# Kernel tuning notes

Measured on AMD Instinct MI355X. Metric: run time of the kernel, lower is better.

The kernel has to match this reference:

```python
import jax, jax.numpy as jnp
import numpy as np

N = 50000      # num nodes
E = 20000      # num hyperedges
NNZ = 800000   # incidence entries
F_IN = 256
HID = [256, 256]
EPS = 1e-5     # BatchNorm eps


def setup_inputs() -> dict:
    key = jax.random.key(0)
    ks = jax.random.split(key, 12)
    x = jax.random.normal(ks[0], (N, F_IN), jnp.float32)
    node_idx = jax.random.randint(ks[1], (NNZ,), 0, N, dtype=jnp.int32)
    edge_idx = jax.random.randint(ks[2], (NNZ,), 0, E, dtype=jnp.int32)
    hyperedge_index = jnp.stack([node_idx, edge_idx])  # [2, NNZ]
    hyperedge_weight = jax.random.uniform(ks[3], (E,), jnp.float32, 0.1, 1.0)
    # layer params: Linear(in, out, bias) + BatchNorm(gamma, beta)
    W1 = jax.random.normal(ks[4], (F_IN, HID[0]), jnp.float32) * (1.0 / np.sqrt(F_IN))
    b1 = jax.random.normal(ks[5], (HID[0],), jnp.float32) * 0.02
    g1 = jnp.ones((HID[0],), jnp.float32)
    be1 = jnp.zeros((HID[0],), jnp.float32)
    W2 = jax.random.normal(ks[6], (HID[0], HID[1]), jnp.float32) * (1.0 / np.sqrt(HID[0]))
    b2 = jax.random.normal(ks[7], (HID[1],), jnp.float32) * 0.02
    g2 = jnp.ones((HID[1],), jnp.float32)
    be2 = jnp.zeros((HID[1],), jnp.float32)
    return dict(x=x, hyperedge_index=hyperedge_index, hyperedge_weight=hyperedge_weight,
                W1=W1, b1=b1, g1=g1, be1=be1, W2=W2, b2=b2, g2=g2, be2=be2)


def _hypergraph_layer(x, node_idx, edge_idx, w_e, W, b, g, be):
    """One HypergraphLayer: HypergraphConv (no attention, heads=1) + BN(train) + ReLU.

    PyG HypergraphConv math: out = D^{-1} H B^{-1} H^T (X Theta) + bias,
    where D_i = sum of incident hyperedge weights, B_e = hyperedge cardinality.
    """
    x = x @ W                                   # [N, F_out] node transform
    # node degree weighted by hyperedge weight
    D = jax.ops.segment_sum(w_e[edge_idx], node_idx, num_segments=N)
    Dinv = jnp.where(D != 0, 1.0 / D, 0.0)
    # hyperedge cardinality
    B = jax.ops.segment_sum(jnp.ones((NNZ,), x.dtype), edge_idx, num_segments=E)
    Binv = jnp.where(B != 0, 1.0 / B, 0.0)
    # node -> edge aggregation: e = B^{-1} H^T x
    e = Binv[:, None] * jax.ops.segment_sum(x[node_idx], edge_idx, num_segments=E)
    # edge -> node aggregation: out = D^{-1} H e
    out = Dinv[:, None] * jax.ops.segment_sum(e[edge_idx], node_idx, num_segments=N)
    out = out + b
    # BatchNorm1d (training mode: biased batch stats over the node dim)
    mu = out.mean(axis=0)
    var = out.var(axis=0)
    out = (out - mu) * jax.lax.rsqrt(var + EPS) * g + be
    return jax.nn.relu(out)                     # dropout p=0.0 -> identity


def reference(x, hyperedge_index, hyperedge_weight, W1, b1, g1, be1, W2, b2, g2, be2):
    node_idx = hyperedge_index[0]
    edge_idx = hyperedge_index[1]
    h = _hypergraph_layer(x, node_idx, edge_idx, hyperedge_weight, W1, b1, g1, be1)
    h = _hypergraph_layer(h, node_idx, edge_idx, hyperedge_weight, W2, b2, g2, be2)
    return h
```

## Files before the change

kernel.cpp:

```cpp
#include <hip/hip_runtime.h>

#define NN     50000
#define NE     20000
#define NNZV   800000
#define FD     256
#define EPSV   1e-5f
#define MPAD   20032
#define NCOPY  32
#define BE     ((NE + 255) / 256)
#define BN     ((NN + 255) / 256)

typedef __attribute__((ext_vector_type(8))) __bf16 bf16x8;
typedef __attribute__((ext_vector_type(4))) __bf16 bf16x4;
typedef __attribute__((ext_vector_type(4))) float f32x4;

__device__ __forceinline__ float b2f(unsigned short u) {
  union { unsigned int i; float f; } z; z.i = ((unsigned)u) << 16; return z.f;
}


__global__ void hg_hist(const int* __restrict__ nidx, const int* __restrict__ eidx,
                        const float* __restrict__ wedge,
                        int* __restrict__ cntc_e, int* __restrict__ cntc_n,
                        float* __restrict__ Daccc,
                        int* __restrict__ rank_e, int* __restrict__ rank_n) {
  int i = blockIdx.x * 256 + threadIdx.x;
  if (i >= NNZV) return;
  int copy = blockIdx.x & (NCOPY - 1);
  int e = eidx[i];
  int n = nidx[i];
  rank_e[i] = atomicAdd(&cntc_e[copy * NE + e], 1);
  rank_n[i] = atomicAdd(&cntc_n[copy * NN + n], 1);
  atomicAdd(&Daccc[copy * NN + n], wedge[e]);
}

__global__ void hg_colreduce_e(int* __restrict__ cntc_e, int* __restrict__ total_e,
                               float* __restrict__ Binv) {
  int e = blockIdx.x * 256 + threadIdx.x;
  if (e >= NE) return;
  int run = 0;
#pragma unroll
  for (int c = 0; c < NCOPY; ++c) {
    int v = cntc_e[c * NE + e];
    cntc_e[c * NE + e] = run;
    run += v;
  }
  total_e[e] = run;
  Binv[e] = run ? 1.0f / (float)run : 0.0f;
}

__global__ void hg_colreduce_n(int* __restrict__ cntc_n, const float* __restrict__ Daccc,
                               int* __restrict__ total_n, float* __restrict__ Dinv) {
  int n = blockIdx.x * 256 + threadIdx.x;
  if (n >= NN) return;
  int run = 0;
  float d = 0.f;
#pragma unroll
  for (int c = 0; c < NCOPY; ++c) {
    int v = cntc_n[c * NN + n];
    cntc_n[c * NN + n] = run;
    run += v;
    d += Daccc[c * NN + n];
  }
  total_n[n] = run;
  Dinv[n] = (d != 0.f) ? 1.0f / d : 0.0f;
}


__global__ void hg_scan1(const int* __restrict__ total_e, const int* __restrict__ total_n,
                         int* __restrict__ part) {
  __shared__ int lds[256];
  int b = blockIdx.x;
  const int* src;
  int n, idx0;
  if (b < BE) { src = total_e; n = NE; idx0 = b * 256; }
  else        { src = total_n; n = NN; idx0 = (b - BE) * 256; }
  int t = threadIdx.x;
  int idx = idx0 + t;
  lds[t] = (idx < n) ? src[idx] : 0;
  for (int d = 128; d > 0; d >>= 1) {
    __syncthreads();
    if (t < d) lds[t] += lds[t + d];
  }
  if (t == 0) part[b] = lds[0];
}

__global__ void hg_scan2(int* __restrict__ part, int* __restrict__ off_e,
                         int* __restrict__ off_n) {
  __shared__ int lds[256];
  int t = threadIdx.x;
  int v = (t < BE) ? part[t] : 0;
  lds[t] = v;
  for (int d = 1; d < 256; d <<= 1) {
    __syncthreads();
    int u = (t >= d) ? lds[t - d] : 0;
    int w = lds[t];
    __syncthreads();
    lds[t] = u + w;
  }
  __syncthreads();
  if (t < BE) part[t] = lds[t] - v;
  if (t == 255) off_e[NE] = lds[255];
  __syncthreads();
  v = (t < BN) ? part[BE + t] : 0;
  lds[t] = v;
  for (int d = 1; d < 256; d <<= 1) {
    __syncthreads();
    int u = (t >= d) ? lds[t - d] : 0;
    int w = lds[t];
    __syncthreads();
    lds[t] = u + w;
  }
  __syncthreads();
  if (t < BN) part[BE + t] = lds[t] - v;
  if (t == 255) off_n[NN] = lds[255];
}

__global__ void hg_scan3(const int* __restrict__ total_e, const int* __restrict__ total_n,
                         const int* __restrict__ part,
                         int* __restrict__ off_e, int* __restrict__ off_n) {
  __shared__ int lds[256];
  int b = blockIdx.x;
  const int* src;
  int* dst;
  int n, idx0;
  if (b < BE) { src = total_e; dst = off_e; n = NE; idx0 = b * 256; }
  else        { src = total_n; dst = off_n; n = NN; idx0 = (b - BE) * 256; }
  int base = part[b];
  int t = threadIdx.x;
  int idx = idx0 + t;
  int v = (idx < n) ? src[idx] : 0;
  lds[t] = v;
  for (int d = 1; d < 256; d <<= 1) {
    __syncthreads();
    int u = (t >= d) ? lds[t - d] : 0;
    int w = lds[t];
    __syncthreads();
    lds[t] = u + w;
  }
  __syncthreads();
  if (idx < n) dst[idx] = base + lds[t] - v;
}

__global__ void hg_addoff(int* __restrict__ cntc_e, int* __restrict__ cntc_n,
                          const int* __restrict__ off_e, const int* __restrict__ off_n) {
  int id = blockIdx.x * 256 + threadIdx.x;
  if (id < NCOPY * NE) {
    cntc_e[id] += off_e[id % NE];
  } else {
    id -= NCOPY * NE;
    if (id < NCOPY * NN) cntc_n[id] += off_n[id % NN];
  }
}

__global__ void hg_scatter(const int* __restrict__ nidx, const int* __restrict__ eidx,
                           const int* __restrict__ cntc_e, const int* __restrict__ cntc_n,
                           const int* __restrict__ rank_e, const int* __restrict__ rank_n,
                           int* __restrict__ mem_e, int* __restrict__ mem_n) {
  int i = blockIdx.x * 256 + threadIdx.x;
  if (i >= NNZV) return;
  int copy = blockIdx.x & (NCOPY - 1);
  int e = eidx[i];
  int n = nidx[i];
  mem_e[cntc_e[copy * NE + e] + rank_e[i]] = n;
  mem_n[cntc_n[copy * NN + n] + rank_n[i]] = e;
}


__global__ void hg_wconv(const float* __restrict__ W1, const float* __restrict__ W2,
                         __bf16* __restrict__ Wt1, __bf16* __restrict__ Wt2) {
  int id = blockIdx.x * 256 + threadIdx.x;
  int n = id >> 8;
  int k = id & 255;
  Wt1[n * FD + k] = (__bf16)W1[k * FD + n];
  Wt2[n * FD + k] = (__bf16)W2[k * FD + n];
}


__global__ void hg_x2bf(const float* __restrict__ X, __bf16* __restrict__ Xbf) {
  int idx = blockIdx.x * 256 + threadIdx.x;
  if (idx >= NN * FD / 4) return;
  float4 v = ((const float4*)X)[idx];
  bf16x4 o = {(__bf16)v.x, (__bf16)v.y, (__bf16)v.z, (__bf16)v.w};
  ((bf16x4*)Xbf)[idx] = o;
}


template<int APPLY>
__global__ __launch_bounds__(256) void
hg_agg_n2e_bf(const __bf16* __restrict__ Xbf, const int* __restrict__ off_e,
              const int* __restrict__ mem_e, const float* __restrict__ Binv,
              const float* __restrict__ scale, const float* __restrict__ shift,
              __bf16* __restrict__ Ebf) {
  int wid = blockIdx.x * 4 + (threadIdx.x >> 6);
  if (wid >= NE) return;
  int lane = threadIdx.x & 63;
  int c = lane * 4;
  float4 sc = {0.f, 0.f, 0.f, 0.f}, sh = {0.f, 0.f, 0.f, 0.f};
  if (APPLY) {
    sc = *(const float4*)(scale + c);
    sh = *(const float4*)(shift + c);
  }
  const unsigned short* Xu = (const unsigned short*)Xbf;
  int lo = off_e[wid], hi = off_e[wid + 1];
  float a0 = 0.f, a1 = 0.f, a2 = 0.f, a3 = 0.f;

#define ACC4(v) do { \
    float f0 = b2f((v).x), f1 = b2f((v).y), f2 = b2f((v).z), f3 = b2f((v).w); \
    if (APPLY) { \
      f0 = fmaxf(fmaf(f0, sc.x, sh.x), 0.f); \
      f1 = fmaxf(fmaf(f1, sc.y, sh.y), 0.f); \
      f2 = fmaxf(fmaf(f2, sc.z, sh.z), 0.f); \
      f3 = fmaxf(fmaf(f3, sc.w, sh.w), 0.f); \
    } \
    a0 += f0; a1 += f1; a2 += f2; a3 += f3; } while (0)

  int m = lo;
  for (; m + 4 <= hi; m += 4) {
    int i0 = mem_e[m], i1 = mem_e[m + 1], i2 = mem_e[m + 2], i3 = mem_e[m + 3];
    ushort4 v0 = *(const ushort4*)(Xu + (size_t)i0 * FD + c);
    ushort4 v1 = *(const ushort4*)(Xu + (size_t)i1 * FD + c);
    ushort4 v2 = *(const ushort4*)(Xu + (size_t)i2 * FD + c);
    ushort4 v3 = *(const ushort4*)(Xu + (size_t)i3 * FD + c);
    ACC4(v0); ACC4(v1); ACC4(v2); ACC4(v3);
  }
  for (; m < hi; ++m) {
    int i0 = mem_e[m];
    ushort4 v0 = *(const ushort4*)(Xu + (size_t)i0 * FD + c);
    ACC4(v0);
  }
  float bi = Binv[wid];
  bf16x4 o = {(__bf16)(a0 * bi), (__bf16)(a1 * bi), (__bf16)(a2 * bi), (__bf16)(a3 * bi)};
  *(bf16x4*)(Ebf + (size_t)wid * FD + c) = o;
}


__global__ void hg_gemm(const __bf16* __restrict__ A, const __bf16* __restrict__ Bt,
                        __bf16* __restrict__ C, int Mrows) {
  int tid = threadIdx.x;
  int w = tid >> 6;
  int l = tid & 63;
  int m0 = blockIdx.x * 64 + w * 16;
  int n0 = blockIdx.y * 16;
  int kbase = (l >> 4) * 8;
  const bf16x8* Ap = (const bf16x8*)(A + (size_t)(m0 + (l & 15)) * FD + kbase);
  const bf16x8* Bp = (const bf16x8*)(Bt + (size_t)(n0 + (l & 15)) * FD + kbase);
  f32x4 acc = {0.f, 0.f, 0.f, 0.f};
#pragma unroll
  for (int ks = 0; ks < 8; ++ks) {
    bf16x8 a = Ap[ks * 4];
    bf16x8 b = Bp[ks * 4];
    acc = __builtin_amdgcn_mfma_f32_16x16x32_bf16(a, b, acc, 0, 0, 0);
  }
  int crow = m0 + (l >> 4) * 4;
  int ccol = n0 + (l & 15);
#pragma unroll
  for (int r = 0; r < 4; ++r) {
    int rr = crow + r;
    if (rr < Mrows) C[(size_t)rr * FD + ccol] = (__bf16)acc[r];
  }
}


__global__ __launch_bounds__(256) void
hg_agg_e2n_bf(const __bf16* __restrict__ eWbf, const int* __restrict__ off_n,
              const int* __restrict__ mem_n, const float* __restrict__ Dinv,
              const float* __restrict__ bias, __bf16* __restrict__ Outbf) {
  int node = blockIdx.x * 4 + (threadIdx.x >> 6);
  if (node >= NN) return;
  int lane = threadIdx.x & 63;
  int c = lane * 4;
  const unsigned short* eWu = (const unsigned short*)eWbf;
  int lo = off_n[node], hi = off_n[node + 1];
  float a0 = 0.f, a1 = 0.f, a2 = 0.f, a3 = 0.f;
  int m = lo;
  for (; m + 4 <= hi; m += 4) {
    int i0 = mem_n[m], i1 = mem_n[m + 1], i2 = mem_n[m + 2], i3 = mem_n[m + 3];
    ushort4 v0 = *(const ushort4*)(eWu + (size_t)i0 * FD + c);
    ushort4 v1 = *(const ushort4*)(eWu + (size_t)i1 * FD + c);
    ushort4 v2 = *(const ushort4*)(eWu + (size_t)i2 * FD + c);
    ushort4 v3 = *(const ushort4*)(eWu + (size_t)i3 * FD + c);
    a0 += b2f(v0.x); a1 += b2f(v0.y); a2 += b2f(v0.z); a3 += b2f(v0.w);
    a0 += b2f(v1.x); a1 += b2f(v1.y); a2 += b2f(v1.z); a3 += b2f(v1.w);
    a0 += b2f(v2.x); a1 += b2f(v2.y); a2 += b2f(v2.z); a3 += b2f(v2.w);
    a0 += b2f(v3.x); a1 += b2f(v3.y); a2 += b2f(v3.z); a3 += b2f(v3.w);
  }
  for (; m < hi; ++m) {
    int i0 = mem_n[m];
    ushort4 v0 = *(const ushort4*)(eWu + (size_t)i0 * FD + c);
    a0 += b2f(v0.x); a1 += b2f(v0.y); a2 += b2f(v0.z); a3 += b2f(v0.w);
  }
  float di = Dinv[node];
  float4 b4 = *(const float4*)(bias + c);
  bf16x4 o = {(__bf16)fmaf(a0, di, b4.x), (__bf16)fmaf(a1, di, b4.y),
              (__bf16)fmaf(a2, di, b4.z), (__bf16)fmaf(a3, di, b4.w)};
  *(bf16x4*)(Outbf + (size_t)node * FD + c) = o;
}


__global__ __launch_bounds__(256) void
hg_stats(const __bf16* __restrict__ Outbf, float* __restrict__ stats) {
  int c = threadIdx.x;
  int rpb = (NN + gridDim.x - 1) / gridDim.x;
  int r0 = blockIdx.x * rpb;
  int r1 = r0 + rpb;
  if (r1 > NN) r1 = NN;
  const unsigned short* Ou = (const unsigned short*)Outbf;
  float s = 0.f, q = 0.f;
  for (int r = r0; r < r1; ++r) {
    float v = b2f(Ou[(size_t)r * FD + c]);
    s += v;
    q = fmaf(v, v, q);
  }
  atomicAdd(&stats[c], s);
  atomicAdd(&stats[FD + c], q);
}


__global__ void hg_bn_finalize(const float* __restrict__ stats, const float* __restrict__ g,
                               const float* __restrict__ be,
                               float* __restrict__ scale, float* __restrict__ shift) {
  int c = threadIdx.x;
  float mu = stats[c] * (1.0f / NN);
  float var = stats[FD + c] * (1.0f / NN) - mu * mu;
  float sc = g[c] * rsqrtf(var + EPSV);
  scale[c] = sc;
  shift[c] = fmaf(-mu, sc, be[c]);
}

__global__ void hg_apply_bf(const __bf16* __restrict__ Outbf, const float* __restrict__ scale,
                            const float* __restrict__ shift, float* __restrict__ H) {
  int idx = blockIdx.x * 256 + threadIdx.x;
  if (idx >= NN * FD / 8) return;
  ushort4 v0 = ((const ushort4*)Outbf)[idx * 2 + 0];
  ushort4 v1 = ((const ushort4*)Outbf)[idx * 2 + 1];
  int c = (idx & (FD / 8 - 1)) * 8;
  float4 sa = *(const float4*)(scale + c);
  float4 sb = *(const float4*)(scale + c + 4);
  float4 ha = *(const float4*)(shift + c);
  float4 hb = *(const float4*)(shift + c + 4);
  float4 o0, o1;
  o0.x = fmaxf(fmaf(b2f(v0.x), sa.x, ha.x), 0.f);
  o0.y = fmaxf(fmaf(b2f(v0.y), sa.y, ha.y), 0.f);
  o0.z = fmaxf(fmaf(b2f(v0.z), sa.z, ha.z), 0.f);
  o0.w = fmaxf(fmaf(b2f(v0.w), sa.w, ha.w), 0.f);
  o1.x = fmaxf(fmaf(b2f(v1.x), sb.x, hb.x), 0.f);
  o1.y = fmaxf(fmaf(b2f(v1.y), sb.y, hb.y), 0.f);
  o1.z = fmaxf(fmaf(b2f(v1.z), sb.z, hb.z), 0.f);
  o1.w = fmaxf(fmaf(b2f(v1.w), sb.w, hb.w), 0.f);
  ((float4*)H)[idx * 2 + 0] = o0;
  ((float4*)H)[idx * 2 + 1] = o1;
}


extern "C" void kernel_launch(void* const* d_in, const int* in_sizes, int n_in,
                              void* d_out, int out_size, void* d_ws, size_t ws_size,
                              hipStream_t stream) {
  const float* x    = (const float*)d_in[0];
  const int*   hei  = (const int*)d_in[1];
  const int*   nidx = hei;
  const int*   eidx = hei + NNZV;
  const float* wedge = (const float*)d_in[2];
  const float* W1  = (const float*)d_in[3];
  const float* b1  = (const float*)d_in[4];
  const float* g1  = (const float*)d_in[5];
  const float* be1 = (const float*)d_in[6];
  const float* W2  = (const float*)d_in[7];
  const float* b2  = (const float*)d_in[8];
  const float* g2  = (const float*)d_in[9];
  const float* be2 = (const float*)d_in[10];
  float* out = (float*)d_out;

  char* base = (char*)d_ws;
  size_t cur = 0;
  auto alloc = [&](size_t bytes) -> void* {
    void* p = base + cur;
    cur += (bytes + 255) & ~(size_t)255;
    return p;
  };
  int*   cntc_e = (int*)alloc((size_t)NCOPY * NE * 4);
  int*   cntc_n = (int*)alloc((size_t)NCOPY * NN * 4);
  float* Daccc  = (float*)alloc((size_t)NCOPY * NN * 4);
  size_t zero_span = cur;
  int*   rank_e = (int*)alloc((size_t)NNZV * 4);
  int*   rank_n = (int*)alloc((size_t)NNZV * 4);
  int*   total_e = (int*)alloc(NE * 4);
  int*   total_n = (int*)alloc(NN * 4);
  int*   part   = (int*)alloc((BE + BN) * 4);
  int*   off_e = (int*)alloc((NE + 1) * 4);
  int*   off_n = (int*)alloc((NN + 1) * 4);
  int*   mem_e = (int*)alloc((size_t)NNZV * 4);
  int*   mem_n = (int*)alloc((size_t)NNZV * 4);
  float* Dinv  = (float*)alloc(NN * 4);
  float* Binv  = (float*)alloc(NE * 4);
  __bf16* Wt1  = (__bf16*)alloc(FD * FD * 2);
  __bf16* Wt2  = (__bf16*)alloc(FD * FD * 2);
  __bf16* Xbf  = (__bf16*)alloc((size_t)NN * FD * 2);
  __bf16* Ebf  = (__bf16*)alloc((size_t)MPAD * FD * 2);
  __bf16* eWbf = (__bf16*)alloc((size_t)MPAD * FD * 2);
  __bf16* Outbf = (__bf16*)alloc((size_t)NN * FD * 2);
  float* stats = (float*)alloc(2 * FD * 4);
  float* scale1 = (float*)alloc(FD * 4);
  float* shift1 = (float*)alloc(FD * 4);
  float* scale2 = (float*)alloc(FD * 4);
  float* shift2 = (float*)alloc(FD * 4);
  if (cur > ws_size) return;

  hipMemsetAsync(base, 0, zero_span, stream);

  hg_hist<<<(NNZV + 255) / 256, 256, 0, stream>>>(nidx, eidx, wedge, cntc_e, cntc_n,
                                                  Daccc, rank_e, rank_n);
  hg_colreduce_e<<<(NE + 255) / 256, 256, 0, stream>>>(cntc_e, total_e, Binv);
  hg_colreduce_n<<<(NN + 255) / 256, 256, 0, stream>>>(cntc_n, Daccc, total_n, Dinv);
  hg_scan1<<<BE + BN, 256, 0, stream>>>(total_e, total_n, part);
  hg_scan2<<<1, 256, 0, stream>>>(part, off_e, off_n);
  hg_scan3<<<BE + BN, 256, 0, stream>>>(total_e, total_n, part, off_e, off_n);
  hg_addoff<<<(NCOPY * (NE + NN) + 255) / 256, 256, 0, stream>>>(cntc_e, cntc_n, off_e, off_n);
  hg_scatter<<<(NNZV + 255) / 256, 256, 0, stream>>>(nidx, eidx, cntc_e, cntc_n,
                                                     rank_e, rank_n, mem_e, mem_n);
  hg_wconv<<<FD, 256, 0, stream>>>(W1, W2, Wt1, Wt2);
  hg_x2bf<<<(NN * FD / 4 + 255) / 256, 256, 0, stream>>>(x, Xbf);

  const int N2E_BLOCKS = (NE + 3) / 4;
  const int E2N_BLOCKS = (NN + 3) / 4;

  hg_agg_n2e_bf<0><<<N2E_BLOCKS, 256, 0, stream>>>(Xbf, off_e, mem_e, Binv,
                                                   nullptr, nullptr, Ebf);
  hg_gemm<<<dim3(MPAD / 64, FD / 16), 256, 0, stream>>>(Ebf, Wt1, eWbf, NE);
  hg_agg_e2n_bf<<<E2N_BLOCKS, 256, 0, stream>>>(eWbf, off_n, mem_n, Dinv, b1, Outbf);
  hipMemsetAsync(stats, 0, 2 * FD * 4, stream);
  hg_stats<<<256, 256, 0, stream>>>(Outbf, stats);
  hg_bn_finalize<<<1, FD, 0, stream>>>(stats, g1, be1, scale1, shift1);

  hg_agg_n2e_bf<1><<<N2E_BLOCKS, 256, 0, stream>>>(Outbf, off_e, mem_e, Binv,
                                                   scale1, shift1, Ebf);
  hg_gemm<<<dim3(MPAD / 64, FD / 16), 256, 0, stream>>>(Ebf, Wt2, eWbf, NE);
  hg_agg_e2n_bf<<<E2N_BLOCKS, 256, 0, stream>>>(eWbf, off_n, mem_n, Dinv, b2, Outbf);
  hipMemsetAsync(stats, 0, 2 * FD * 4, stream);
  hg_stats<<<256, 256, 0, stream>>>(Outbf, stats);
  hg_bn_finalize<<<1, FD, 0, stream>>>(stats, g2, be2, scale2, shift2);
  hg_apply_bf<<<(NN * FD / 8 + 255) / 256, 256, 0, stream>>>(Outbf, scale2, shift2, out);
}
```

Baseline: 688.6 us.

## Build CSR with LDS-packed 16-bit histograms and compute degrees on the fly

Replaces the global-atomic multi-copy histogram with a per-block LDS histogram that packs two 16-bit counters per word, over 128 contiguous chunks. Ranks are stored as 16-bit values, and the per-copy offset is added inside scatter, which removes the memset and addoff kernels. Binv and Dinv are no longer precomputed: they come from the CSR segment length and a running sum of hyperedge weights inside the aggregation kernels. The aggregation loops are also unrolled to 8 gathers. The trade-off is a few extra wedge gathers in the e2n kernel, and 16-bit counters that overflow if any chunk sees 65536 or more repeats of one id.

```diff
diff --git a/kernel.cpp b/kernel.cpp
--- a/kernel.cpp
+++ b/kernel.cpp
@@ -6,7 +6,11 @@
 #define FD     256
 #define EPSV   1e-5f
 #define MPAD   20032
-#define NCOPY  32
+#define NCPY   128
+#define EPB    (NNZV / NCPY)
+#define HEC    (NE / 2)
+#define HNC    (NN / 2)
+#define HTC    (HEC + HNC)
 #define BE     ((NE + 255) / 256)
 #define BN     ((NN + 255) / 256)
 
@@ -19,51 +23,49 @@
 }
 
 
-__global__ void hg_hist(const int* __restrict__ nidx, const int* __restrict__ eidx,
-                        const float* __restrict__ wedge,
-                        int* __restrict__ cntc_e, int* __restrict__ cntc_n,
-                        float* __restrict__ Daccc,
-                        int* __restrict__ rank_e, int* __restrict__ rank_n) {
-  int i = blockIdx.x * 256 + threadIdx.x;
-  if (i >= NNZV) return;
-  int copy = blockIdx.x & (NCOPY - 1);
-  int e = eidx[i];
-  int n = nidx[i];
-  rank_e[i] = atomicAdd(&cntc_e[copy * NE + e], 1);
-  rank_n[i] = atomicAdd(&cntc_n[copy * NN + n], 1);
-  atomicAdd(&Daccc[copy * NN + n], wedge[e]);
-}
-
-__global__ void hg_colreduce_e(int* __restrict__ cntc_e, int* __restrict__ total_e,
-                               float* __restrict__ Binv) {
-  int e = blockIdx.x * 256 + threadIdx.x;
-  if (e >= NE) return;
-  int run = 0;
-#pragma unroll
-  for (int c = 0; c < NCOPY; ++c) {
-    int v = cntc_e[c * NE + e];
-    cntc_e[c * NE + e] = run;
+__global__ __launch_bounds__(256) void
+hg_histlds(const int* __restrict__ nidx, const int* __restrict__ eidx,
+           unsigned* __restrict__ cntc,
+           unsigned short* __restrict__ rank_e16, unsigned short* __restrict__ rank_n16) {
+  __shared__ unsigned hist[HTC];
+  int b = blockIdx.x, t = threadIdx.x;
+  for (int j = t; j < HTC; j += 256) hist[j] = 0;
+  __syncthreads();
+  int i0 = b * EPB;
+  for (int i = i0 + t; i < i0 + EPB; i += 256) {
+    int e = eidx[i];
+    int n = nidx[i];
+    unsigned se = (e & 1) * 16;
+    unsigned sn = (n & 1) * 16;
+    unsigned oe = atomicAdd(&hist[e >> 1], 1u << se);
+    unsigned on = atomicAdd(&hist[HEC + (n >> 1)], 1u << sn);
+    rank_e16[i] = (unsigned short)((oe >> se) & 0xffffu);
+    rank_n16[i] = (unsigned short)((on >> sn) & 0xffffu);
+  }
+  __syncthreads();
+  unsigned* dst = cntc + (size_t)b * HTC;
+  for (int j = t; j < HTC; j += 256) dst[j] = hist[j];
+}
+
+__global__ void hg_colreduce(unsigned* __restrict__ cntc,
+                             int* __restrict__ total_e, int* __restrict__ total_n) {
+  int j = blockIdx.x * 256 + threadIdx.x;
+  if (j >= HTC) return;
+  unsigned run = 0;
+#pragma unroll 4
+  for (int c = 0; c < NCPY; ++c) {
+    unsigned v = cntc[(size_t)c * HTC + j];
+    cntc[(size_t)c * HTC + j] = run;
     run += v;
   }
-  total_e[e] = run;
-  Binv[e] = run ? 1.0f / (float)run : 0.0f;
-}
-
-__global__ void hg_colreduce_n(int* __restrict__ cntc_n, const float* __restrict__ Daccc,
-                               int* __restrict__ total_n, float* __restrict__ Dinv) {
-  int n = blockIdx.x * 256 + threadIdx.x;
-  if (n >= NN) return;
-  int run = 0;
-  float d = 0.f;
-#pragma unroll
-  for (int c = 0; c < NCOPY; ++c) {
-    int v = cntc_n[c * NN + n];
-    cntc_n[c * NN + n] = run;
-    run += v;
-    d += Daccc[c * NN + n];
-  }
-  total_n[n] = run;
-  Dinv[n] = (d != 0.f) ? 1.0f / d : 0.0f;
+  if (j < HEC) {
+    total_e[2 * j]     = run & 0xffffu;
+    total_e[2 * j + 1] = run >> 16;
+  } else {
+    int k = j - HEC;
+    total_n[2 * k]     = run & 0xffffu;
+    total_n[2 * k + 1] = run >> 16;
+  }
 }
 
 
@@ -142,28 +144,24 @@
   if (idx < n) dst[idx] = base + lds[t] - v;
 }
 
-__global__ void hg_addoff(int* __restrict__ cntc_e, int* __restrict__ cntc_n,
-                          const int* __restrict__ off_e, const int* __restrict__ off_n) {
-  int id = blockIdx.x * 256 + threadIdx.x;
-  if (id < NCOPY * NE) {
-    cntc_e[id] += off_e[id % NE];
-  } else {
-    id -= NCOPY * NE;
-    if (id < NCOPY * NN) cntc_n[id] += off_n[id % NN];
-  }
-}
 
 __global__ void hg_scatter(const int* __restrict__ nidx, const int* __restrict__ eidx,
-                           const int* __restrict__ cntc_e, const int* __restrict__ cntc_n,
-                           const int* __restrict__ rank_e, const int* __restrict__ rank_n,
+                           const unsigned* __restrict__ cntc,
+                           const unsigned short* __restrict__ rank_e16,
+                           const unsigned short* __restrict__ rank_n16,
+                           const int* __restrict__ off_e, const int* __restrict__ off_n,
                            int* __restrict__ mem_e, int* __restrict__ mem_n) {
   int i = blockIdx.x * 256 + threadIdx.x;
   if (i >= NNZV) return;
-  int copy = blockIdx.x & (NCOPY - 1);
+  unsigned copy = (unsigned)i / EPB;
   int e = eidx[i];
   int n = nidx[i];
-  mem_e[cntc_e[copy * NE + e] + rank_e[i]] = n;
-  mem_n[cntc_n[copy * NN + n] + rank_n[i]] = e;
+  unsigned be = cntc[(size_t)copy * HTC + (e >> 1)];
+  be = (be >> ((e & 1) * 16)) & 0xffffu;
+  unsigned bn = cntc[(size_t)copy * HTC + HEC + (n >> 1)];
+  bn = (bn >> ((n & 1) * 16)) & 0xffffu;
+  mem_e[off_e[e] + be + rank_e16[i]] = n;
+  mem_n[off_n[n] + bn + rank_n16[i]] = e;
 }
 
 
@@ -189,7 +187,7 @@
 template<int APPLY>
 __global__ __launch_bounds__(256) void
 hg_agg_n2e_bf(const __bf16* __restrict__ Xbf, const int* __restrict__ off_e,
-              const int* __restrict__ mem_e, const float* __restrict__ Binv,
+              const int* __restrict__ mem_e,
               const float* __restrict__ scale, const float* __restrict__ shift,
               __bf16* __restrict__ Ebf) {
   int wid = blockIdx.x * 4 + (threadIdx.x >> 6);
@@ -216,6 +214,20 @@
     a0 += f0; a1 += f1; a2 += f2; a3 += f3; } while (0)
 
   int m = lo;
+  for (; m + 8 <= hi; m += 8) {
+    int i0 = mem_e[m],     i1 = mem_e[m + 1], i2 = mem_e[m + 2], i3 = mem_e[m + 3];
+    int i4 = mem_e[m + 4], i5 = mem_e[m + 5], i6 = mem_e[m + 6], i7 = mem_e[m + 7];
+    ushort4 v0 = *(const ushort4*)(Xu + (size_t)i0 * FD + c);
+    ushort4 v1 = *(const ushort4*)(Xu + (size_t)i1 * FD + c);
+    ushort4 v2 = *(const ushort4*)(Xu + (size_t)i2 * FD + c);
+    ushort4 v3 = *(const ushort4*)(Xu + (size_t)i3 * FD + c);
+    ushort4 v4 = *(const ushort4*)(Xu + (size_t)i4 * FD + c);
+    ushort4 v5 = *(const ushort4*)(Xu + (size_t)i5 * FD + c);
+    ushort4 v6 = *(const ushort4*)(Xu + (size_t)i6 * FD + c);
+    ushort4 v7 = *(const ushort4*)(Xu + (size_t)i7 * FD + c);
+    ACC4(v0); ACC4(v1); ACC4(v2); ACC4(v3);
+    ACC4(v4); ACC4(v5); ACC4(v6); ACC4(v7);
+  }
   for (; m + 4 <= hi; m += 4) {
     int i0 = mem_e[m], i1 = mem_e[m + 1], i2 = mem_e[m + 2], i3 = mem_e[m + 3];
     ushort4 v0 = *(const ushort4*)(Xu + (size_t)i0 * FD + c);
@@ -229,7 +241,8 @@
     ushort4 v0 = *(const ushort4*)(Xu + (size_t)i0 * FD + c);
     ACC4(v0);
   }
-  float bi = Binv[wid];
+  int cnt = hi - lo;
+  float bi = cnt ? 1.0f / (float)cnt : 0.0f;
   bf16x4 o = {(__bf16)(a0 * bi), (__bf16)(a1 * bi), (__bf16)(a2 * bi), (__bf16)(a3 * bi)};
   *(bf16x4*)(Ebf + (size_t)wid * FD + c) = o;
 }
@@ -264,7 +277,7 @@
 
 __global__ __launch_bounds__(256) void
 hg_agg_e2n_bf(const __bf16* __restrict__ eWbf, const int* __restrict__ off_n,
-              const int* __restrict__ mem_n, const float* __restrict__ Dinv,
+              const int* __restrict__ mem_n, const float* __restrict__ wedge,
               const float* __restrict__ bias, __bf16* __restrict__ Outbf) {
   int node = blockIdx.x * 4 + (threadIdx.x >> 6);
   if (node >= NN) return;
@@ -273,24 +286,37 @@
   const unsigned short* eWu = (const unsigned short*)eWbf;
   int lo = off_n[node], hi = off_n[node + 1];
   float a0 = 0.f, a1 = 0.f, a2 = 0.f, a3 = 0.f;
+  float dw = 0.f;
   int m = lo;
-  for (; m + 4 <= hi; m += 4) {
-    int i0 = mem_n[m], i1 = mem_n[m + 1], i2 = mem_n[m + 2], i3 = mem_n[m + 3];
+  for (; m + 8 <= hi; m += 8) {
+    int i0 = mem_n[m],     i1 = mem_n[m + 1], i2 = mem_n[m + 2], i3 = mem_n[m + 3];
+    int i4 = mem_n[m + 4], i5 = mem_n[m + 5], i6 = mem_n[m + 6], i7 = mem_n[m + 7];
     ushort4 v0 = *(const ushort4*)(eWu + (size_t)i0 * FD + c);
     ushort4 v1 = *(const ushort4*)(eWu + (size_t)i1 * FD + c);
     ushort4 v2 = *(const ushort4*)(eWu + (size_t)i2 * FD + c);
     ushort4 v3 = *(const ushort4*)(eWu + (size_t)i3 * FD + c);
+    ushort4 v4 = *(const ushort4*)(eWu + (size_t)i4 * FD + c);
+    ushort4 v5 = *(const ushort4*)(eWu + (size_t)i5 * FD + c);
+    ushort4 v6 = *(const ushort4*)(eWu + (size_t)i6 * FD + c);
+    ushort4 v7 = *(const ushort4*)(eWu + (size_t)i7 * FD + c);
+    dw += wedge[i0] + wedge[i1] + wedge[i2] + wedge[i3]
+        + wedge[i4] + wedge[i5] + wedge[i6] + wedge[i7];
     a0 += b2f(v0.x); a1 += b2f(v0.y); a2 += b2f(v0.z); a3 += b2f(v0.w);
     a0 += b2f(v1.x); a1 += b2f(v1.y); a2 += b2f(v1.z); a3 += b2f(v1.w);
     a0 += b2f(v2.x); a1 += b2f(v2.y); a2 += b2f(v2.z); a3 += b2f(v2.w);
     a0 += b2f(v3.x); a1 += b2f(v3.y); a2 += b2f(v3.z); a3 += b2f(v3.w);
+    a0 += b2f(v4.x); a1 += b2f(v4.y); a2 += b2f(v4.z); a3 += b2f(v4.w);
+    a0 += b2f(v5.x); a1 += b2f(v5.y); a2 += b2f(v5.z); a3 += b2f(v5.w);
+    a0 += b2f(v6.x); a1 += b2f(v6.y); a2 += b2f(v6.z); a3 += b2f(v6.w);
+    a0 += b2f(v7.x); a1 += b2f(v7.y); a2 += b2f(v7.z); a3 += b2f(v7.w);
   }
   for (; m < hi; ++m) {
     int i0 = mem_n[m];
     ushort4 v0 = *(const ushort4*)(eWu + (size_t)i0 * FD + c);
+    dw += wedge[i0];
     a0 += b2f(v0.x); a1 += b2f(v0.y); a2 += b2f(v0.z); a3 += b2f(v0.w);
   }
-  float di = Dinv[node];
+  float di = (dw != 0.f) ? 1.0f / dw : 0.0f;
   float4 b4 = *(const float4*)(bias + c);
   bf16x4 o = {(__bf16)fmaf(a0, di, b4.x), (__bf16)fmaf(a1, di, b4.y),
               (__bf16)fmaf(a2, di, b4.z), (__bf16)fmaf(a3, di, b4.w)};
@@ -378,21 +404,16 @@
     cur += (bytes + 255) & ~(size_t)255;
     return p;
   };
-  int*   cntc_e = (int*)alloc((size_t)NCOPY * NE * 4);
-  int*   cntc_n = (int*)alloc((size_t)NCOPY * NN * 4);
-  float* Daccc  = (float*)alloc((size_t)NCOPY * NN * 4);
-  size_t zero_span = cur;
-  int*   rank_e = (int*)alloc((size_t)NNZV * 4);
-  int*   rank_n = (int*)alloc((size_t)NNZV * 4);
+  unsigned* cntc = (unsigned*)alloc((size_t)NCPY * HTC * 4);
+  unsigned short* rank_e16 = (unsigned short*)alloc((size_t)NNZV * 2);
+  unsigned short* rank_n16 = (unsigned short*)alloc((size_t)NNZV * 2);
   int*   total_e = (int*)alloc(NE * 4);
   int*   total_n = (int*)alloc(NN * 4);
-  int*   part   = (int*)alloc((BE + BN) * 4);
+  int*   part  = (int*)alloc((BE + BN) * 4);
   int*   off_e = (int*)alloc((NE + 1) * 4);
   int*   off_n = (int*)alloc((NN + 1) * 4);
   int*   mem_e = (int*)alloc((size_t)NNZV * 4);
   int*   mem_n = (int*)alloc((size_t)NNZV * 4);
-  float* Dinv  = (float*)alloc(NN * 4);
-  float* Binv  = (float*)alloc(NE * 4);
   __bf16* Wt1  = (__bf16*)alloc(FD * FD * 2);
   __bf16* Wt2  = (__bf16*)alloc(FD * FD * 2);
   __bf16* Xbf  = (__bf16*)alloc((size_t)NN * FD * 2);
@@ -406,36 +427,29 @@
   float* shift2 = (float*)alloc(FD * 4);
   if (cur > ws_size) return;
 
-  hipMemsetAsync(base, 0, zero_span, stream);
-
-  hg_hist<<<(NNZV + 255) / 256, 256, 0, stream>>>(nidx, eidx, wedge, cntc_e, cntc_n,
-                                                  Daccc, rank_e, rank_n);
-  hg_colreduce_e<<<(NE + 255) / 256, 256, 0, stream>>>(cntc_e, total_e, Binv);
-  hg_colreduce_n<<<(NN + 255) / 256, 256, 0, stream>>>(cntc_n, Daccc, total_n, Dinv);
+  hg_histlds<<<NCPY, 256, 0, stream>>>(nidx, eidx, cntc, rank_e16, rank_n16);
+  hg_colreduce<<<(HTC + 255) / 256, 256, 0, stream>>>(cntc, total_e, total_n);
   hg_scan1<<<BE + BN, 256, 0, stream>>>(total_e, total_n, part);
   hg_scan2<<<1, 256, 0, stream>>>(part, off_e, off_n);
   hg_scan3<<<BE + BN, 256, 0, stream>>>(total_e, total_n, part, off_e, off_n);
-  hg_addoff<<<(NCOPY * (NE + NN) + 255) / 256, 256, 0, stream>>>(cntc_e, cntc_n, off_e, off_n);
-  hg_scatter<<<(NNZV + 255) / 256, 256, 0, stream>>>(nidx, eidx, cntc_e, cntc_n,
-                                                     rank_e, rank_n, mem_e, mem_n);
+  hg_scatter<<<(NNZV + 255) / 256, 256, 0, stream>>>(nidx, eidx, cntc, rank_e16, rank_n16,
+                                                     off_e, off_n, mem_e, mem_n);
   hg_wconv<<<FD, 256, 0, stream>>>(W1, W2, Wt1, Wt2);
   hg_x2bf<<<(NN * FD / 4 + 255) / 256, 256, 0, stream>>>(x, Xbf);
 
   const int N2E_BLOCKS = (NE + 3) / 4;
   const int E2N_BLOCKS = (NN + 3) / 4;
 
-  hg_agg_n2e_bf<0><<<N2E_BLOCKS, 256, 0, stream>>>(Xbf, off_e, mem_e, Binv,
-                                                   nullptr, nullptr, Ebf);
+  hg_agg_n2e_bf<0><<<N2E_BLOCKS, 256, 0, stream>>>(Xbf, off_e, mem_e, nullptr, nullptr, Ebf);
   hg_gemm<<<dim3(MPAD / 64, FD / 16), 256, 0, stream>>>(Ebf, Wt1, eWbf, NE);
-  hg_agg_e2n_bf<<<E2N_BLOCKS, 256, 0, stream>>>(eWbf, off_n, mem_n, Dinv, b1, Outbf);
+  hg_agg_e2n_bf<<<E2N_BLOCKS, 256, 0, stream>>>(eWbf, off_n, mem_n, wedge, b1, Outbf);
   hipMemsetAsync(stats, 0, 2 * FD * 4, stream);
   hg_stats<<<256, 256, 0, stream>>>(Outbf, stats);
   hg_bn_finalize<<<1, FD, 0, stream>>>(stats, g1, be1, scale1, shift1);
 
-  hg_agg_n2e_bf<1><<<N2E_BLOCKS, 256, 0, stream>>>(Outbf, off_e, mem_e, Binv,
-                                                   scale1, shift1, Ebf);
+  hg_agg_n2e_bf<1><<<N2E_BLOCKS, 256, 0, stream>>>(Outbf, off_e, mem_e, scale1, shift1, Ebf);
   hg_gemm<<<dim3(MPAD / 64, FD / 16), 256, 0, stream>>>(Ebf, Wt2, eWbf, NE);
-  hg_agg_e2n_bf<<<E2N_BLOCKS, 256, 0, stream>>>(eWbf, off_n, mem_n, Dinv, b2, Outbf);
+  hg_agg_e2n_bf<<<E2N_BLOCKS, 256, 0, stream>>>(eWbf, off_n, mem_n, wedge, b2, Outbf);
   hipMemsetAsync(stats, 0, 2 * FD * 4, stream);
   hg_stats<<<256, 256, 0, stream>>>(Outbf, stats);
   hg_bn_finalize<<<1, FD, 0, stream>>>(stats, g2, be2, scale2, shift2);
```

After: 619.7 us. 1.11x faster.
